# Kernel optimization log

Measured on AMD Instinct MI355X. Metric: run time of the kernel, lower is better.

## Reference

```python
import jax, jax.numpy as jnp
import numpy as np

B, N, M, D = 8, 512, 64, 128
H = 64  # mlp_hidden_dim


def setup_inputs() -> dict:
    key = jax.random.key(0)
    ks = jax.random.split(key, 10)
    op_emb = jax.random.normal(ks[0], (B, N, D), dtype=jnp.float32)
    machine_emb = jax.random.normal(ks[1], (B, M, D), dtype=jnp.float32)
    edge_emb = jax.random.normal(ks[2], (B, N, M, D), dtype=jnp.float32)
    action_mask = jax.random.randint(ks[3], (B, N, M), 0, 2) > 0
    s1 = 1.0 / np.sqrt(3 * D)
    s2 = 1.0 / np.sqrt(H)
    W1 = jax.random.uniform(ks[4], (3 * D, H), jnp.float32, -s1, s1)
    b1 = jax.random.uniform(ks[5], (H,), jnp.float32, -s1, s1)
    W2 = jax.random.uniform(ks[6], (H, H), jnp.float32, -s2, s2)
    b2 = jax.random.uniform(ks[7], (H,), jnp.float32, -s2, s2)
    W3 = jax.random.uniform(ks[8], (H, 1), jnp.float32, -s2, s2)
    b3 = jax.random.uniform(ks[9], (1,), jnp.float32, -s2, s2)
    return {"op_emb": op_emb, "machine_emb": machine_emb, "edge_emb": edge_emb,
            "action_mask": action_mask,
            "W1": W1, "b1": b1, "W2": W2, "b2": b2, "W3": W3, "b3": b3}


def reference(op_emb, machine_emb, edge_emb, action_mask, W1, b1, W2, b2, W3, b3):
    # Split first linear over the three concat chunks to avoid materializing
    # the (B,N,M,3D) concat tensor (same math as cat -> Linear).
    Wo, Wm, We = W1[:D], W1[D:2 * D], W1[2 * D:]
    h = (jnp.einsum('bnd,dh->bnh', op_emb, Wo)[:, :, None, :]
         + jnp.einsum('bmd,dh->bmh', machine_emb, Wm)[:, None, :, :]
         + jnp.einsum('bnmd,dh->bnmh', edge_emb, We) + b1)  # (B,N,M,H)
    h = jax.nn.relu(h)
    h = jax.nn.relu(h @ W2 + b2)
    scores = (h @ W3 + b3)[..., 0]  # (B,N,M)
    scores = jnp.where(action_mask, scores, -jnp.inf)
    return jax.nn.log_softmax(scores.reshape(B, N * M), axis=-1)
```

## Files before the change

### kernel.cpp

```cpp
#include <hip/hip_runtime.h>
#include <math.h>

#define Bb 8
#define Nn 512
#define Mm 64
#define Dd 128
#define Hh 64
#define NEG_BIG (-1.0e30f)

typedef __bf16 bf16x8 __attribute__((ext_vector_type(8)));
typedef float  f32x4  __attribute__((ext_vector_type(4)));

#define WS_WEB   0u
#define WS_W2B   16384u
#define WS_CWSF  24576u
#define WS_AOP   155648u
#define WS_SCORE 1204224u
#define WS_PART  2252800u

__global__ __launch_bounds__(256) void prep_kernel(
    const float* __restrict__ W1, const float* __restrict__ W2,
    const float* __restrict__ op_emb, const float* __restrict__ machine_emb,
    const float* __restrict__ b1, char* __restrict__ ws)
{
    if (blockIdx.x < 48) {
        __bf16* WeB = (__bf16*)(ws + WS_WEB);
        __bf16* W2B = (__bf16*)(ws + WS_W2B);
        int idx = blockIdx.x * 256 + threadIdx.x;
        if (idx < 8192) {
            int fid = idx >> 9, rem = idx & 511;
            int lane = rem >> 3, j = rem & 7;
            int t = fid >> 2, ks = fid & 3;
            int q = lane >> 4, ln = lane & 15;
            int d = ks * 32 + q * 8 + j;
            int h = t * 16 + ln;
            WeB[idx] = (__bf16)W1[(size_t)(2 * Dd + d) * Hh + h];
        } else {
            int i2 = idx - 8192;
            int fid = i2 >> 9, rem = i2 & 511;
            int lane = rem >> 3, j = rem & 7;
            int t = fid >> 1, ks = fid & 1;
            int q = lane >> 4, ln = lane & 15;
            int k = ks * 32 + q * 8 + j;
            int h = t * 16 + ln;
            W2B[i2] = (__bf16)W2[(size_t)k * Hh + h];
        }
        return;
    }
    float* CwsF = (float*)(ws + WS_CWSF);
    float* Aop  = (float*)(ws + WS_AOP);
    const int bid = (blockIdx.x - 48) * 4 + (threadIdx.x >> 6);
    const int h = threadIdx.x & 63;
    if (bid < Bb * Mm) {
        const float* mg = machine_emb + (size_t)bid * Dd;
        const float* Wm = W1 + (size_t)Dd * Hh;
        float acc = b1[h];
#pragma unroll 8
        for (int d = 0; d < Dd; ++d) acc = fmaf(mg[d], Wm[d * Hh + h], acc);
        int b = bid >> 6, m = bid & 63;
        int wq = m >> 4, q = (m >> 2) & 3, r = m & 3;
        int t = h >> 4, ln = h & 15;
        CwsF[((((b * 4 + wq) * 4 + t) * 64) + (q * 16 + ln)) * 4 + r] = acc;
    } else {
        const int bn = bid - Bb * Mm;
        const float* og = op_emb + (size_t)bn * Dd;
        float acc = 0.f;
#pragma unroll 8
        for (int d = 0; d < Dd; ++d) acc = fmaf(og[d], W1[d * Hh + h], acc);
        Aop[(size_t)bn * Hh + h] = acc;
    }
}

__global__ __launch_bounds__(256, 2) void main_kernel(
    const float* __restrict__ edge_emb, const int* __restrict__ mask,
    const float* __restrict__ b2, const float* __restrict__ W3,
    const float* __restrict__ b3, char* __restrict__ ws)
{
    __shared__ __bf16 sH1[Mm * 72];
    __shared__ float  sRed[8];

    float* scores = (float*)(ws + WS_SCORE);
    float* part   = (float*)(ws + WS_PART);

    const int tid  = threadIdx.x;
    const int lane = tid & 63;
    const int w    = tid >> 6;
    const int q    = lane >> 4;
    const int ln   = lane & 15;
    const int bn   = blockIdx.x;
    const int b    = bn >> 9;

    const float* Eg = edge_emb + (size_t)bn * (Mm * Dd) + (w * 16 + ln) * Dd + q * 8;
    float4 raw[8];
#pragma unroll
    for (int ks = 0; ks < 4; ++ks) {
        raw[2 * ks]     = *(const float4*)&Eg[ks * 32];
        raw[2 * ks + 1] = *(const float4*)&Eg[ks * 32 + 4];
    }
    bf16x8 weF[16], w2F[8];
    {
        const bf16x8* WeB = (const bf16x8*)(ws + WS_WEB);
        const bf16x8* W2B = (const bf16x8*)(ws + WS_W2B);
#pragma unroll
        for (int f = 0; f < 16; ++f) weF[f] = WeB[f * 64 + lane];
#pragma unroll
        for (int f = 0; f < 8; ++f)  w2F[f] = W2B[f * 64 + lane];
    }
    f32x4 cv[4];
    {
        const f32x4* CwsF = (const f32x4*)(ws + WS_CWSF) + (size_t)b * 1024;
#pragma unroll
        for (int t = 0; t < 4; ++t) cv[t] = CwsF[(w * 4 + t) * 64 + lane];
    }
    const float* Aop = (const float*)(ws + WS_AOP) + (size_t)bn * Hh;
    float aopv[4];
#pragma unroll
    for (int t = 0; t < 4; ++t) aopv[t] = Aop[t * 16 + ln];
    const int4 mk = *(const int4*)&mask[(size_t)bn * Mm + w * 16 + q * 4];
    float b2v[4], w3v[4];
#pragma unroll
    for (int t = 0; t < 4; ++t) { b2v[t] = b2[t * 16 + ln]; w3v[t] = W3[t * 16 + ln]; }
    const float bias3 = b3[0];

    bf16x8 af[4];
#pragma unroll
    for (int ks = 0; ks < 4; ++ks) {
        float4 lo = raw[2 * ks], hi = raw[2 * ks + 1];
        bf16x8 a;
        a[0] = (__bf16)lo.x; a[1] = (__bf16)lo.y; a[2] = (__bf16)lo.z; a[3] = (__bf16)lo.w;
        a[4] = (__bf16)hi.x; a[5] = (__bf16)hi.y; a[6] = (__bf16)hi.z; a[7] = (__bf16)hi.w;
        af[ks] = a;
    }

    f32x4 acc[4];
#pragma unroll
    for (int t = 0; t < 4; ++t) {
        acc[t][0] = cv[t][0] + aopv[t]; acc[t][1] = cv[t][1] + aopv[t];
        acc[t][2] = cv[t][2] + aopv[t]; acc[t][3] = cv[t][3] + aopv[t];
    }
#pragma unroll
    for (int t = 0; t < 4; ++t)
#pragma unroll
        for (int ks = 0; ks < 4; ++ks)
            acc[t] = __builtin_amdgcn_mfma_f32_16x16x32_bf16(af[ks], weF[t * 4 + ks], acc[t], 0, 0, 0);

#pragma unroll
    for (int t = 0; t < 4; ++t)
#pragma unroll
        for (int r = 0; r < 4; ++r)
            sH1[(w * 16 + q * 4 + r) * 72 + t * 16 + ln] = (__bf16)fmaxf(acc[t][r], 0.f);

    bf16x8 a2[2];
#pragma unroll
    for (int ks = 0; ks < 2; ++ks)
        a2[ks] = *(const bf16x8*)&sH1[(w * 16 + ln) * 72 + ks * 32 + q * 8];
    f32x4 c2[4];
#pragma unroll
    for (int t = 0; t < 4; ++t) c2[t] = (f32x4){0.f, 0.f, 0.f, 0.f};
#pragma unroll
    for (int t = 0; t < 4; ++t)
#pragma unroll
        for (int ks = 0; ks < 2; ++ks)
            c2[t] = __builtin_amdgcn_mfma_f32_16x16x32_bf16(a2[ks], w2F[t * 2 + ks], c2[t], 0, 0, 0);

    float p[4] = {0.f, 0.f, 0.f, 0.f};
#pragma unroll
    for (int t = 0; t < 4; ++t)
#pragma unroll
        for (int r = 0; r < 4; ++r)
            p[r] += fmaxf(c2[t][r] + b2v[t], 0.f) * w3v[t];
#pragma unroll
    for (int r = 0; r < 4; ++r) {
        p[r] += __shfl_xor(p[r], 1, 64);
        p[r] += __shfl_xor(p[r], 2, 64);
        p[r] += __shfl_xor(p[r], 4, 64);
        p[r] += __shfl_xor(p[r], 8, 64);
    }
    float m_loc = NEG_BIG, l_loc = 0.f;
    const int m0 = w * 16 + q * 4;
    {
        const int mkv[4] = {mk.x, mk.y, mk.z, mk.w};
        float vv[4];
#pragma unroll
        for (int r = 0; r < 4; ++r) {
            float v = p[r] + bias3;
            vv[r] = mkv[r] ? v : NEG_BIG;
            if (mkv[r]) {
                float mn = fmaxf(m_loc, v);
                l_loc = l_loc * expf(m_loc - mn) + expf(v - mn);
                m_loc = mn;
            }
        }
        if (ln == 0) {
            float4 o; o.x = vv[0]; o.y = vv[1]; o.z = vv[2]; o.w = vv[3];
            *(float4*)&scores[(size_t)bn * Mm + m0] = o;
        }
    }
#pragma unroll
    for (int off = 16; off <= 32; off <<= 1) {
        float mo = __shfl_xor(m_loc, off, 64);
        float lo2 = __shfl_xor(l_loc, off, 64);
        float mn = fmaxf(m_loc, mo);
        l_loc = l_loc * expf(m_loc - mn) + lo2 * expf(mo - mn);
        m_loc = mn;
    }
    if (lane == 0) { sRed[w * 2] = m_loc; sRed[w * 2 + 1] = l_loc; }
    __syncthreads();
    if (tid == 0) {
        float gm = sRed[0], gl = sRed[1];
#pragma unroll
        for (int k = 1; k < 4; ++k) {
            float mo = sRed[k * 2], lo2 = sRed[k * 2 + 1];
            float mn = fmaxf(gm, mo);
            gl = gl * expf(gm - mn) + lo2 * expf(mo - mn);
            gm = mn;
        }
        float2 o; o.x = gm; o.y = gl;
        *(float2*)&part[bn * 2] = o;
    }
}

__global__ __launch_bounds__(256) void lsm_apply_kernel(
    const char* __restrict__ ws, float* __restrict__ out)
{
    const float4* s4 = (const float4*)(ws + WS_SCORE);
    const float* part = (const float*)(ws + WS_PART);
    __shared__ float sComb[8];
    __shared__ float sCC;
    const int tid = threadIdx.x;
    const int b = blockIdx.x >> 5;
    {
        float4 v = *(const float4*)&part[(size_t)b * 1024 + tid * 4];
        float mn = fmaxf(v.x, v.z);
        float m_loc = mn;
        float l_loc = v.y * expf(v.x - mn) + v.w * expf(v.z - mn);
#pragma unroll
        for (int off = 1; off < 64; off <<= 1) {
            float mo = __shfl_xor(m_loc, off, 64);
            float lo2 = __shfl_xor(l_loc, off, 64);
            float nm = fmaxf(m_loc, mo);
            l_loc = l_loc * expf(m_loc - nm) + lo2 * expf(mo - nm);
            m_loc = nm;
        }
        if ((tid & 63) == 0) { sComb[(tid >> 6) * 2] = m_loc; sComb[(tid >> 6) * 2 + 1] = l_loc; }
    }
    __syncthreads();
    if (tid == 0) {
        float gm = sComb[0], gl = sComb[1];
#pragma unroll
        for (int k = 1; k < 4; ++k) {
            float mo = sComb[k * 2], lo2 = sComb[k * 2 + 1];
            float mn = fmaxf(gm, mo);
            gl = gl * expf(gm - mn) + lo2 * expf(mo - mn);
            gm = mn;
        }
        sCC = gm + logf(gl);
    }
    __syncthreads();
    const float c = sCC;
    const int i = blockIdx.x * 256 + tid;
    float4 v = s4[i];
    v.x -= c; v.y -= c; v.z -= c; v.w -= c;
    ((float4*)out)[i] = v;
}

extern "C" void kernel_launch(void* const* d_in, const int* in_sizes, int n_in,
                              void* d_out, int out_size, void* d_ws, size_t ws_size,
                              hipStream_t stream)
{
    const float* op_emb      = (const float*)d_in[0];
    const float* machine_emb = (const float*)d_in[1];
    const float* edge_emb    = (const float*)d_in[2];
    const int*   mask        = (const int*)  d_in[3];
    const float* W1 = (const float*)d_in[4];
    const float* b1 = (const float*)d_in[5];
    const float* W2 = (const float*)d_in[6];
    const float* b2 = (const float*)d_in[7];
    const float* W3 = (const float*)d_in[8];
    const float* b3 = (const float*)d_in[9];
    char* ws = (char*)d_ws;

    prep_kernel<<<48 + 1152, 256, 0, stream>>>(W1, W2, op_emb, machine_emb, b1, ws);
    main_kernel<<<Bb * Nn, 256, 0, stream>>>(edge_emb, mask, b2, W3, b3, ws);
    lsm_apply_kernel<<<256, 256, 0, stream>>>(ws, (float*)d_out);
}
```

Before: 237.2 us.

## Make main kernel persistent over batches with double-buffered global-to-LDS edge prefetch

Each main-kernel block now loops over all 8 batch entries for one n index instead of handling a single (b,n) tile, and the grid shrinks from 4096 to 512 blocks. Edge-embedding tiles are streamed with asynchronous global_load_lds into a two-stage LDS buffer, so the next tile's fetch overlaps the current tile's MFMA work. Weight fragments are loaded once per block instead of once per tile. The block-level softmax partial reduction and its __syncthreads are dropped: each wave writes its own partial, and the apply kernel merges eight partials per thread. The costs are a large LDS footprint, which may limit occupancy, and only 512 blocks to keep the GPU's compute units busy.

```diff
diff --git a/kernel.cpp b/kernel.cpp
--- a/kernel.cpp
+++ b/kernel.cpp
@@ -8,6 +8,9 @@
 #define Hh 64
 #define NEG_BIG (-1.0e30f)
 
+#define SEGF 260
+#define BUFF (8 * SEGF)
+
 typedef __bf16 bf16x8 __attribute__((ext_vector_type(8)));
 typedef float  f32x4  __attribute__((ext_vector_type(4)));
 
@@ -17,6 +20,10 @@
 #define WS_AOP   155648u
 #define WS_SCORE 1204224u
 #define WS_PART  2252800u
+
+#define GLOAD_LDS(gp, lp) __builtin_amdgcn_global_load_lds( \
+    (const __attribute__((address_space(1))) void*)(gp),    \
+    (__attribute__((address_space(3))) void*)(lp), 16, 0, 0)
 
 __global__ __launch_bounds__(256) void prep_kernel(
     const float* __restrict__ W1, const float* __restrict__ W2,
@@ -76,27 +83,34 @@
     const float* __restrict__ b2, const float* __restrict__ W3,
     const float* __restrict__ b3, char* __restrict__ ws)
 {
+    __shared__ float  sEdge[4 * 2 * BUFF];
     __shared__ __bf16 sH1[Mm * 72];
-    __shared__ float  sRed[8];
 
     float* scores = (float*)(ws + WS_SCORE);
     float* part   = (float*)(ws + WS_PART);
+    const float* CwsF = (const float*)(ws + WS_CWSF);
+    const float* Aop  = (const float*)(ws + WS_AOP);
 
     const int tid  = threadIdx.x;
     const int lane = tid & 63;
     const int w    = tid >> 6;
     const int q    = lane >> 4;
     const int ln   = lane & 15;
-    const int bn   = blockIdx.x;
-    const int b    = bn >> 9;
-
-    const float* Eg = edge_emb + (size_t)bn * (Mm * Dd) + (w * 16 + ln) * Dd + q * 8;
-    float4 raw[8];
-#pragma unroll
-    for (int ks = 0; ks < 4; ++ks) {
-        raw[2 * ks]     = *(const float4*)&Eg[ks * 32];
-        raw[2 * ks + 1] = *(const float4*)&Eg[ks * 32 + 4];
-    }
+    const int i    = blockIdx.x;
+    const int wu   = __builtin_amdgcn_readfirstlane(w);
+
+    const float* e0 = edge_emb + (size_t)i * (Mm * Dd) + w * 2048 + lane * 4;
+#define TILE_STRIDE ((size_t)512 * Mm * Dd)
+
+    {
+        float* d0 = &sEdge[(wu * 2 + 0) * BUFF];
+        float* d1 = &sEdge[(wu * 2 + 1) * BUFF];
+#pragma unroll
+        for (int s = 0; s < 8; ++s) GLOAD_LDS(e0 + s * 256, d0 + s * SEGF);
+#pragma unroll
+        for (int s = 0; s < 8; ++s) GLOAD_LDS(e0 + TILE_STRIDE + s * 256, d1 + s * SEGF);
+    }
+
     bf16x8 weF[16], w2F[8];
     {
         const bf16x8* WeB = (const bf16x8*)(ws + WS_WEB);
@@ -106,80 +120,99 @@
 #pragma unroll
         for (int f = 0; f < 8; ++f)  w2F[f] = W2B[f * 64 + lane];
     }
-    f32x4 cv[4];
-    {
-        const f32x4* CwsF = (const f32x4*)(ws + WS_CWSF) + (size_t)b * 1024;
-#pragma unroll
-        for (int t = 0; t < 4; ++t) cv[t] = CwsF[(w * 4 + t) * 64 + lane];
-    }
-    const float* Aop = (const float*)(ws + WS_AOP) + (size_t)bn * Hh;
-    float aopv[4];
-#pragma unroll
-    for (int t = 0; t < 4; ++t) aopv[t] = Aop[t * 16 + ln];
-    const int4 mk = *(const int4*)&mask[(size_t)bn * Mm + w * 16 + q * 4];
     float b2v[4], w3v[4];
 #pragma unroll
     for (int t = 0; t < 4; ++t) { b2v[t] = b2[t * 16 + ln]; w3v[t] = W3[t * 16 + ln]; }
     const float bias3 = b3[0];
 
-    bf16x8 af[4];
-#pragma unroll
-    for (int ks = 0; ks < 4; ++ks) {
-        float4 lo = raw[2 * ks], hi = raw[2 * ks + 1];
-        bf16x8 a;
-        a[0] = (__bf16)lo.x; a[1] = (__bf16)lo.y; a[2] = (__bf16)lo.z; a[3] = (__bf16)lo.w;
-        a[4] = (__bf16)hi.x; a[5] = (__bf16)hi.y; a[6] = (__bf16)hi.z; a[7] = (__bf16)hi.w;
-        af[ks] = a;
-    }
-
-    f32x4 acc[4];
-#pragma unroll
-    for (int t = 0; t < 4; ++t) {
-        acc[t][0] = cv[t][0] + aopv[t]; acc[t][1] = cv[t][1] + aopv[t];
-        acc[t][2] = cv[t][2] + aopv[t]; acc[t][3] = cv[t][3] + aopv[t];
-    }
-#pragma unroll
-    for (int t = 0; t < 4; ++t)
-#pragma unroll
-        for (int ks = 0; ks < 4; ++ks)
-            acc[t] = __builtin_amdgcn_mfma_f32_16x16x32_bf16(af[ks], weF[t * 4 + ks], acc[t], 0, 0, 0);
-
-#pragma unroll
-    for (int t = 0; t < 4; ++t)
-#pragma unroll
-        for (int r = 0; r < 4; ++r)
-            sH1[(w * 16 + q * 4 + r) * 72 + t * 16 + ln] = (__bf16)fmaxf(acc[t][r], 0.f);
-
-    bf16x8 a2[2];
-#pragma unroll
-    for (int ks = 0; ks < 2; ++ks)
-        a2[ks] = *(const bf16x8*)&sH1[(w * 16 + ln) * 72 + ks * 32 + q * 8];
-    f32x4 c2[4];
-#pragma unroll
-    for (int t = 0; t < 4; ++t) c2[t] = (f32x4){0.f, 0.f, 0.f, 0.f};
-#pragma unroll
-    for (int t = 0; t < 4; ++t)
+    const int rdoff = (ln >> 1) * SEGF + (ln & 1) * 128 + q * 8;
+
+#pragma unroll
+    for (int g = 0; g < Bb; ++g) {
+        const int bn = g * 512 + i;
+        const int buf = g & 1;
+        const float* ldsrd = &sEdge[(wu * 2 + buf) * BUFF];
+
+        __builtin_amdgcn_s_waitcnt(0x0F7A);
+
+        f32x4 lo[4], hi[4];
+#pragma unroll
+        for (int ks = 0; ks < 4; ++ks) {
+            lo[ks] = *(const f32x4*)&ldsrd[rdoff + ks * 32];
+            hi[ks] = *(const f32x4*)&ldsrd[rdoff + ks * 32 + 4];
+        }
+        bf16x8 af[4];
+#pragma unroll
+        for (int ks = 0; ks < 4; ++ks) {
+            bf16x8 a;
+            a[0] = (__bf16)lo[ks][0]; a[1] = (__bf16)lo[ks][1];
+            a[2] = (__bf16)lo[ks][2]; a[3] = (__bf16)lo[ks][3];
+            a[4] = (__bf16)hi[ks][0]; a[5] = (__bf16)hi[ks][1];
+            a[6] = (__bf16)hi[ks][2]; a[7] = (__bf16)hi[ks][3];
+            af[ks] = a;
+        }
+
+        f32x4 cv[4];
+#pragma unroll
+        for (int t = 0; t < 4; ++t)
+            cv[t] = *(const f32x4*)&CwsF[((((g * 4 + w) * 4 + t) * 64) + lane) * 4];
+        float aopv[4];
+#pragma unroll
+        for (int t = 0; t < 4; ++t) aopv[t] = Aop[(size_t)bn * Hh + t * 16 + ln];
+        const int4 mk = *(const int4*)&mask[(size_t)bn * Mm + w * 16 + q * 4];
+
+        if (g + 2 < Bb) {
+            float* dst = &sEdge[(wu * 2 + buf) * BUFF];
+            const float* src = e0 + (size_t)(g + 2) * TILE_STRIDE;
+#pragma unroll
+            for (int s = 0; s < 8; ++s) GLOAD_LDS(src + s * 256, dst + s * SEGF);
+        }
+
+        f32x4 acc[4];
+#pragma unroll
+        for (int t = 0; t < 4; ++t) acc[t] = (f32x4){0.f, 0.f, 0.f, 0.f};
+#pragma unroll
+        for (int t = 0; t < 4; ++t)
+#pragma unroll
+            for (int ks = 0; ks < 4; ++ks)
+                acc[t] = __builtin_amdgcn_mfma_f32_16x16x32_bf16(af[ks], weF[t * 4 + ks], acc[t], 0, 0, 0);
+
+#pragma unroll
+        for (int t = 0; t < 4; ++t)
+#pragma unroll
+            for (int r = 0; r < 4; ++r)
+                sH1[(w * 16 + q * 4 + r) * 72 + t * 16 + ln] =
+                    (__bf16)fmaxf(acc[t][r] + aopv[t] + cv[t][r], 0.f);
+
+        bf16x8 a2[2];
 #pragma unroll
         for (int ks = 0; ks < 2; ++ks)
-            c2[t] = __builtin_amdgcn_mfma_f32_16x16x32_bf16(a2[ks], w2F[t * 2 + ks], c2[t], 0, 0, 0);
-
-    float p[4] = {0.f, 0.f, 0.f, 0.f};
-#pragma unroll
-    for (int t = 0; t < 4; ++t)
-#pragma unroll
-        for (int r = 0; r < 4; ++r)
-            p[r] += fmaxf(c2[t][r] + b2v[t], 0.f) * w3v[t];
-#pragma unroll
-    for (int r = 0; r < 4; ++r) {
-        p[r] += __shfl_xor(p[r], 1, 64);
-        p[r] += __shfl_xor(p[r], 2, 64);
-        p[r] += __shfl_xor(p[r], 4, 64);
-        p[r] += __shfl_xor(p[r], 8, 64);
-    }
-    float m_loc = NEG_BIG, l_loc = 0.f;
-    const int m0 = w * 16 + q * 4;
-    {
+            a2[ks] = *(const bf16x8*)&sH1[(w * 16 + ln) * 72 + ks * 32 + q * 8];
+        f32x4 c2[4];
+#pragma unroll
+        for (int t = 0; t < 4; ++t) c2[t] = (f32x4){0.f, 0.f, 0.f, 0.f};
+#pragma unroll
+        for (int t = 0; t < 4; ++t)
+#pragma unroll
+            for (int ks = 0; ks < 2; ++ks)
+                c2[t] = __builtin_amdgcn_mfma_f32_16x16x32_bf16(a2[ks], w2F[t * 2 + ks], c2[t], 0, 0, 0);
+
+        float p[4] = {0.f, 0.f, 0.f, 0.f};
+#pragma unroll
+        for (int t = 0; t < 4; ++t)
+#pragma unroll
+            for (int r = 0; r < 4; ++r)
+                p[r] += fmaxf(c2[t][r] + b2v[t], 0.f) * w3v[t];
+#pragma unroll
+        for (int r = 0; r < 4; ++r) {
+            p[r] += __shfl_xor(p[r], 1, 64);
+            p[r] += __shfl_xor(p[r], 2, 64);
+            p[r] += __shfl_xor(p[r], 4, 64);
+            p[r] += __shfl_xor(p[r], 8, 64);
+        }
+        const int m0 = w * 16 + q * 4;
         const int mkv[4] = {mk.x, mk.y, mk.z, mk.w};
+        float m_loc = NEG_BIG, l_loc = 0.f;
         float vv[4];
 #pragma unroll
         for (int r = 0; r < 4; ++r) {
@@ -195,28 +228,18 @@
             float4 o; o.x = vv[0]; o.y = vv[1]; o.z = vv[2]; o.w = vv[3];
             *(float4*)&scores[(size_t)bn * Mm + m0] = o;
         }
-    }
-#pragma unroll
-    for (int off = 16; off <= 32; off <<= 1) {
-        float mo = __shfl_xor(m_loc, off, 64);
-        float lo2 = __shfl_xor(l_loc, off, 64);
-        float mn = fmaxf(m_loc, mo);
-        l_loc = l_loc * expf(m_loc - mn) + lo2 * expf(mo - mn);
-        m_loc = mn;
-    }
-    if (lane == 0) { sRed[w * 2] = m_loc; sRed[w * 2 + 1] = l_loc; }
-    __syncthreads();
-    if (tid == 0) {
-        float gm = sRed[0], gl = sRed[1];
-#pragma unroll
-        for (int k = 1; k < 4; ++k) {
-            float mo = sRed[k * 2], lo2 = sRed[k * 2 + 1];
-            float mn = fmaxf(gm, mo);
-            gl = gl * expf(gm - mn) + lo2 * expf(mo - mn);
-            gm = mn;
-        }
-        float2 o; o.x = gm; o.y = gl;
-        *(float2*)&part[bn * 2] = o;
+#pragma unroll
+        for (int off = 16; off <= 32; off <<= 1) {
+            float mo = __shfl_xor(m_loc, off, 64);
+            float lo2 = __shfl_xor(l_loc, off, 64);
+            float mn = fmaxf(m_loc, mo);
+            l_loc = l_loc * expf(m_loc - mn) + lo2 * expf(mo - mn);
+            m_loc = mn;
+        }
+        if (lane == 0) {
+            float2 o; o.x = m_loc; o.y = l_loc;
+            *(float2*)&part[((size_t)bn * 4 + w) * 2] = o;
+        }
     }
 }
 
@@ -230,10 +253,15 @@
     const int tid = threadIdx.x;
     const int b = blockIdx.x >> 5;
     {
-        float4 v = *(const float4*)&part[(size_t)b * 1024 + tid * 4];
-        float mn = fmaxf(v.x, v.z);
-        float m_loc = mn;
-        float l_loc = v.y * expf(v.x - mn) + v.w * expf(v.z - mn);
+        float m_loc = NEG_BIG, l_loc = 0.f;
+        const float* pb = &part[(size_t)b * 4096];
+#pragma unroll
+        for (int k = 0; k < 8; ++k) {
+            float2 p = *(const float2*)&pb[(tid * 8 + k) * 2];
+            float mn = fmaxf(m_loc, p.x);
+            l_loc = l_loc * expf(m_loc - mn) + p.y * expf(p.x - mn);
+            m_loc = mn;
+        }
 #pragma unroll
         for (int off = 1; off < 64; off <<= 1) {
             float mo = __shfl_xor(m_loc, off, 64);
@@ -258,10 +286,10 @@
     }
     __syncthreads();
     const float c = sCC;
-    const int i = blockIdx.x * 256 + tid;
-    float4 v = s4[i];
+    const int idx = blockIdx.x * 256 + tid;
+    float4 v = s4[idx];
     v.x -= c; v.y -= c; v.z -= c; v.w -= c;
-    ((float4*)out)[i] = v;
+    ((float4*)out)[idx] = v;
 }
 
 extern "C" void kernel_launch(void* const* d_in, const int* in_sizes, int n_in,
@@ -281,6 +309,6 @@
     char* ws = (char*)d_ws;
 
     prep_kernel<<<48 + 1152, 256, 0, stream>>>(W1, W2, op_emb, machine_emb, b1, ws);
-    main_kernel<<<Bb * Nn, 256, 0, stream>>>(edge_emb, mask, b2, W3, b3, ws);
+    main_kernel<<<Nn, 256, 0, stream>>>(edge_emb, mask, b2, W3, b3, ws);
     lsm_apply_kernel<<<256, 256, 0, stream>>>(ws, (float*)d_out);
 }
```

After: 229.7 us. 3.2% less time.
